# Kernel optimization log

Hardware: AMD Instinct MI355X
Metric: run time of the kernel (lower is better)

The kernel has to match this reference:

```python
import jax, jax.numpy as jnp
import numpy as np

D_MODEL = 1024
N_EXPERTS = 16384
N_HEADS = 8
TOP_K = 16
D_KEY = 128
N_SUB = int(np.sqrt(N_EXPERTS))  # 128
BN_EPS = 1e-5
RMS_EPS = 1e-6


def setup_inputs() -> dict:
    key = jax.random.key(0)
    ks = jax.random.split(key, 12)
    b, t = 2, 512
    hk = N_HEADS * D_KEY  # 1024
    s = 0.02
    return {
        "x": jax.random.normal(ks[0], (b, t, D_MODEL), dtype=jnp.float32),
        "wq": jax.random.normal(ks[1], (hk, D_MODEL), dtype=jnp.float32) * s,
        "bq": jnp.zeros((hk,), dtype=jnp.float32),
        "bn_w": jnp.ones((hk,), dtype=jnp.float32),
        "bn_b": jnp.zeros((hk,), dtype=jnp.float32),
        "bn_mean": jnp.zeros((hk,), dtype=jnp.float32),
        "bn_var": jnp.ones((hk,), dtype=jnp.float32),
        "sub_keys": jax.random.normal(ks[2], (2, N_SUB, D_KEY // 2), dtype=jnp.float32),
        "expert_weights": jax.random.normal(ks[3], (N_EXPERTS, D_KEY), dtype=jnp.float32),
        "wo": jax.random.normal(ks[4], (D_MODEL, hk), dtype=jnp.float32) * s,
        "bo": jnp.zeros((D_MODEL,), dtype=jnp.float32),
        "in_proj_w": jax.random.normal(ks[5], (3 * D_MODEL, D_MODEL), dtype=jnp.float32) * s,
        "in_proj_b": jnp.zeros((3 * D_MODEL,), dtype=jnp.float32),
        "attn_ow": jax.random.normal(ks[6], (D_MODEL, D_MODEL), dtype=jnp.float32) * s,
        "attn_ob": jnp.zeros((D_MODEL,), dtype=jnp.float32),
        "rms_w": jnp.ones((D_MODEL,), dtype=jnp.float32),
    }


def reference(x, wq, bq, bn_w, bn_b, bn_mean, bn_var, sub_keys, expert_weights,
              wo, bo, in_proj_w, in_proj_b, attn_ow, attn_ob, rms_w):
    b, t, d = x.shape
    h, dk = N_HEADS, D_KEY

    # ---- PEER query path ----
    q = jnp.einsum('btd,ed->bte', x, wq) + bq                       # (b,t,h*dk)
    # BatchNorm1d in eval mode with running stats
    q = (q - bn_mean) * jax.lax.rsqrt(bn_var + BN_EPS) * bn_w + bn_b
    q = q.reshape(b, t, h, dk)

    # ---- product-key top-k retrieval ----
    q1, q2 = q[..., : dk // 2], q[..., dk // 2 :]
    s1 = jnp.einsum('bthc,nc->bthn', q1, sub_keys[0])               # (b,t,h,N_SUB)
    s2 = jnp.einsum('bthc,nc->bthn', q2, sub_keys[1])
    # cartesian add; flat index = i1*N_SUB + i2 (matches torch view)
    scores = (s1[..., :, None] + s2[..., None, :]).reshape(b, t, h, N_SUB * N_SUB)
    _, idx = jax.lax.top_k(scores, TOP_K)                           # (b,t,h,k)

    # ---- gather experts, router softmax, weighted sum ----
    ew = expert_weights[idx]                                        # (b,t,h,k,dk)
    sim = jnp.einsum('bthd,bthkd->bthk', q, ew)
    rw = jax.nn.softmax(sim, axis=-1)
    out = jnp.einsum('bthk,bthkd->bthd', rw, ew).reshape(b, t, h * dk)
    out = jnp.einsum('bte,de->btd', out, wo) + bo                   # (b,t,d)

    # ---- multihead self-attention (torch nn.MultiheadAttention semantics) ----
    hd = d // h
    qkv = jnp.einsum('btd,ed->bte', x, in_proj_w) + in_proj_b       # (b,t,3d)
    qa, ka, va = jnp.split(qkv, 3, axis=-1)
    def heads(z):
        return z.reshape(b, t, h, hd).transpose(0, 2, 1, 3)         # (b,h,t,hd)
    qa, ka, va = heads(qa), heads(ka), heads(va)
    att = jax.nn.softmax(jnp.einsum('bhqe,bhke->bhqk', qa, ka) / np.sqrt(hd), axis=-1)
    ao = jnp.einsum('bhqk,bhke->bhqe', att, va).transpose(0, 2, 1, 3).reshape(b, t, d)
    ao = jnp.einsum('btd,ed->bte', ao, attn_ow) + attn_ob
    attn_weights = att.mean(axis=1)                                 # (b,t,t), averaged over heads

    # ---- residual + RMSNorm ----
    y = x + out + ao
    y = y * jax.lax.rsqrt(jnp.mean(y * y, axis=-1, keepdims=True) + RMS_EPS) * rms_w
    return y, attn_weights
```

## Files before the change

### kernel.cpp

```cpp
#include <hip/hip_runtime.h>
#include <hip/hip_bf16.h>
#include <math.h>

typedef __attribute__((ext_vector_type(8))) short bf16x8;
typedef __attribute__((ext_vector_type(4))) float f32x4;

__device__ inline short f2bf(float f) {
    __hip_bfloat16 h = __float2bfloat16(f);
    return *reinterpret_cast<short*>(&h);
}

__device__ inline unsigned int obits(float f) {
    unsigned int u = __float_as_uint(f);
    return (u & 0x80000000u) ? ~u : (u | 0x80000000u);
}

__global__ __launch_bounds__(256) void gemm_mfma64(
    const float* __restrict__ A, long lda, long sAb, long sAh,
    const float* __restrict__ B, long ldb, long sBb, long sBh,
    float* __restrict__ C, long ldc, long sCb, long sCh,
    int K, const float* __restrict__ bias, float scale, int hDiv)
{
    int bz = blockIdx.z;
    int bb = bz / hDiv, hh = bz % hDiv;
    A += bb * sAb + hh * sAh;
    B += bb * sBb + hh * sBh;
    C += bb * sCb + hh * sCh;
    int bm = blockIdx.y * 64, bn = blockIdx.x * 64;

    __shared__ __align__(16) short Asub[2][2048];
    __shared__ __align__(16) short Bsub[2][2048];

    int tid = threadIdx.x;
    int lane = tid & 63;
    int wave = tid >> 6;
    int wr = wave >> 1, wc = wave & 1;
    int l15 = lane & 15, l4 = lane >> 4;

    f32x4 acc[2][2] = {};

    int sr = tid >> 2;
    int sq = tid & 3;
    const float* gA = A + (long)(bm + sr) * lda + sq * 8;
    const float* gB = B + (long)(bn + sr) * ldb + sq * 8;
    int woff = (sr >> 4) * 512 + sq * 128 + (sr & 15) * 8;

    float4 a0 = *(const float4*)(gA);
    float4 a1 = *(const float4*)(gA + 4);
    float4 b0 = *(const float4*)(gB);
    float4 b1 = *(const float4*)(gB + 4);
    {
        bf16x8 ua, ub;
        ua[0]=f2bf(a0.x); ua[1]=f2bf(a0.y); ua[2]=f2bf(a0.z); ua[3]=f2bf(a0.w);
        ua[4]=f2bf(a1.x); ua[5]=f2bf(a1.y); ua[6]=f2bf(a1.z); ua[7]=f2bf(a1.w);
        ub[0]=f2bf(b0.x); ub[1]=f2bf(b0.y); ub[2]=f2bf(b0.z); ub[3]=f2bf(b0.w);
        ub[4]=f2bf(b1.x); ub[5]=f2bf(b1.y); ub[6]=f2bf(b1.z); ub[7]=f2bf(b1.w);
        *(bf16x8*)(Asub[0] + woff) = ua;
        *(bf16x8*)(Bsub[0] + woff) = ub;
    }
    if (K > 32) {
        a0 = *(const float4*)(gA + 32);
        a1 = *(const float4*)(gA + 36);
        b0 = *(const float4*)(gB + 32);
        b1 = *(const float4*)(gB + 36);
    }
    __syncthreads();

    int p = 0;
    for (int k0 = 0; k0 < K; k0 += 32) {
        bf16x8 af[2], bfr[2];
#pragma unroll
        for (int mi = 0; mi < 2; mi++)
            af[mi] = *(const bf16x8*)(Asub[p] + (wr * 2 + mi) * 512 + l4 * 128 + l15 * 8);
#pragma unroll
        for (int ni = 0; ni < 2; ni++)
            bfr[ni] = *(const bf16x8*)(Bsub[p] + (wc * 2 + ni) * 512 + l4 * 128 + l15 * 8);

        if (k0 + 32 < K) {
            bf16x8 ua, ub;
            ua[0]=f2bf(a0.x); ua[1]=f2bf(a0.y); ua[2]=f2bf(a0.z); ua[3]=f2bf(a0.w);
            ua[4]=f2bf(a1.x); ua[5]=f2bf(a1.y); ua[6]=f2bf(a1.z); ua[7]=f2bf(a1.w);
            ub[0]=f2bf(b0.x); ub[1]=f2bf(b0.y); ub[2]=f2bf(b0.z); ub[3]=f2bf(b0.w);
            ub[4]=f2bf(b1.x); ub[5]=f2bf(b1.y); ub[6]=f2bf(b1.z); ub[7]=f2bf(b1.w);
            *(bf16x8*)(Asub[p ^ 1] + woff) = ua;
            *(bf16x8*)(Bsub[p ^ 1] + woff) = ub;
            if (k0 + 64 < K) {
                a0 = *(const float4*)(gA + k0 + 64);
                a1 = *(const float4*)(gA + k0 + 68);
                b0 = *(const float4*)(gB + k0 + 64);
                b1 = *(const float4*)(gB + k0 + 68);
            }
        }

#pragma unroll
        for (int mi = 0; mi < 2; mi++)
#pragma unroll
            for (int ni = 0; ni < 2; ni++)
                acc[mi][ni] = __builtin_amdgcn_mfma_f32_16x16x32_bf16(
                    af[mi], bfr[ni], acc[mi][ni], 0, 0, 0);
        __syncthreads();
        p ^= 1;
    }

#pragma unroll
    for (int ni = 0; ni < 2; ni++) {
        int c = bn + wc * 32 + ni * 16 + l15;
        float bv = bias ? bias[c] : 0.f;
#pragma unroll
        for (int mi = 0; mi < 2; mi++) {
            int r0 = bm + wr * 32 + mi * 16 + l4 * 4;
#pragma unroll
            for (int e = 0; e < 4; e++)
                C[(long)(r0 + e) * ldc + c] = acc[mi][ni][e] * scale + bv;
        }
    }
}

__global__ __launch_bounds__(256) void sgemm_qproj(
    const float* __restrict__ A, const float* __restrict__ W,
    float* __restrict__ Q,
    const float* __restrict__ bq, const float* __restrict__ bn_w,
    const float* __restrict__ bn_b, const float* __restrict__ bn_mean,
    const float* __restrict__ bn_var)
{
    int bm = blockIdx.y * 64, bn = blockIdx.x * 64;
    __shared__ float As[32][64];
    __shared__ float Bs[32][64];
    int tid = threadIdx.x;
    int tx = tid & 15, ty = tid >> 4;
    int r = tid >> 2, q4 = tid & 3;
    float acc[4][4] = {{0.f}};

    const float* ga = A + (long)(bm + r) * 1024 + q4 * 8;
    const float* gb = W + (long)(bn + r) * 1024 + q4 * 8;

    float4 a0 = *(const float4*)(ga);
    float4 a1 = *(const float4*)(ga + 4);
    float4 b0 = *(const float4*)(gb);
    float4 b1 = *(const float4*)(gb + 4);

    for (int k0 = 0; k0 < 1024; k0 += 32) {
        __syncthreads();
        As[q4 * 8 + 0][r] = a0.x; As[q4 * 8 + 1][r] = a0.y;
        As[q4 * 8 + 2][r] = a0.z; As[q4 * 8 + 3][r] = a0.w;
        As[q4 * 8 + 4][r] = a1.x; As[q4 * 8 + 5][r] = a1.y;
        As[q4 * 8 + 6][r] = a1.z; As[q4 * 8 + 7][r] = a1.w;
        Bs[q4 * 8 + 0][r] = b0.x; Bs[q4 * 8 + 1][r] = b0.y;
        Bs[q4 * 8 + 2][r] = b0.z; Bs[q4 * 8 + 3][r] = b0.w;
        Bs[q4 * 8 + 4][r] = b1.x; Bs[q4 * 8 + 5][r] = b1.y;
        Bs[q4 * 8 + 6][r] = b1.z; Bs[q4 * 8 + 7][r] = b1.w;
        if (k0 + 32 < 1024) {
            a0 = *(const float4*)(ga + k0 + 32);
            a1 = *(const float4*)(ga + k0 + 36);
            b0 = *(const float4*)(gb + k0 + 32);
            b1 = *(const float4*)(gb + k0 + 36);
        }
        __syncthreads();
#pragma unroll
        for (int kk = 0; kk < 32; kk++) {
            float4 av = *(const float4*)&As[kk][ty * 4];
            float4 bv = *(const float4*)&Bs[kk][tx * 4];
            float a[4] = {av.x, av.y, av.z, av.w};
            float b[4] = {bv.x, bv.y, bv.z, bv.w};
#pragma unroll
            for (int i = 0; i < 4; i++)
#pragma unroll
                for (int j = 0; j < 4; j++)
                    acc[i][j] = fmaf(a[i], b[j], acc[i][j]);
        }
    }

#pragma unroll
    for (int j = 0; j < 4; j++) {
        int n = bn + tx * 4 + j;
        float s = rsqrtf(bn_var[n] + 1e-5f) * bn_w[n];
        float base = bq[n] - bn_mean[n];
        float bb = bn_b[n];
#pragma unroll
        for (int i = 0; i < 4; i++) {
            long m = bm + ty * 4 + i;
            Q[m * 1024 + n] = (acc[i][j] + base) * s + bb;
        }
    }
}

__global__ __launch_bounds__(256) void transpose_va(
    const float* __restrict__ qkv, float* __restrict__ vat)
{
    int z = blockIdx.z;
    int b = z >> 3, h = z & 7;
    int k0 = blockIdx.x * 32, n0 = blockIdx.y * 32;
    __shared__ float tile[32][33];
    int tx = threadIdx.x & 31, ty = threadIdx.x >> 5;
    const float* src = qkv + 2048 + (long)b * 1572864 + (long)h * 128;
#pragma unroll
    for (int i = 0; i < 4; i++)
        tile[ty + 8 * i][tx] = src[(long)(k0 + ty + 8 * i) * 3072 + n0 + tx];
    __syncthreads();
    float* dst = vat + (long)z * 65536;
#pragma unroll
    for (int i = 0; i < 4; i++)
        dst[(long)(n0 + ty + 8 * i) * 512 + k0 + tx] = tile[tx][ty + 8 * i];
}

__global__ __launch_bounds__(128) void peer_kernel(
    const float* __restrict__ q,
    const float* __restrict__ sub_keys,
    const float* __restrict__ ew,
    float* __restrict__ out)
{
    int th = blockIdx.x;
    int tid = threadIdx.x;

    __shared__ __align__(16) float qrow[128];
    __shared__ __align__(16) float s1s[128];
    __shared__ __align__(16) float s2s[128];
    __shared__ __align__(16) unsigned long long cks[256];
    __shared__ float tv1[16], tv2[16];
    __shared__ int   ti1[16], ti2[16];
    __shared__ int   part[100];
    __shared__ int   eid[16];
    __shared__ float simv[16];
    __shared__ float rw[16];

    qrow[tid] = q[(long)th * 128 + tid];
    __syncthreads();

    float a1 = 0.f, a2 = 0.f;
    {
        const float4* k1 = (const float4*)(sub_keys + tid * 64);
        const float4* k2 = (const float4*)(sub_keys + 8192 + tid * 64);
#pragma unroll 4
        for (int c = 0; c < 16; c++) {
            float4 q1 = *(const float4*)&qrow[4 * c];
            float4 q2 = *(const float4*)&qrow[64 + 4 * c];
            float4 v1 = k1[c], v2 = k2[c];
            a1 = fmaf(q1.x, v1.x, a1); a1 = fmaf(q1.y, v1.y, a1);
            a1 = fmaf(q1.z, v1.z, a1); a1 = fmaf(q1.w, v1.w, a1);
            a2 = fmaf(q2.x, v2.x, a2); a2 = fmaf(q2.y, v2.y, a2);
            a2 = fmaf(q2.z, v2.z, a2); a2 = fmaf(q2.w, v2.w, a2);
        }
    }
    s1s[tid] = a1;
    s2s[tid] = a2;
    __syncthreads();

    {
        int r1 = 0, r2 = 0;
        for (int j = 0; j < 128; j += 4) {
            float4 a = *(const float4*)&s1s[j];
            float4 b = *(const float4*)&s2s[j];
            r1 += (a.x > a1) || (a.x == a1 && j + 0 < tid);
            r1 += (a.y > a1) || (a.y == a1 && j + 1 < tid);
            r1 += (a.z > a1) || (a.z == a1 && j + 2 < tid);
            r1 += (a.w > a1) || (a.w == a1 && j + 3 < tid);
            r2 += (b.x > a2) || (b.x == a2 && j + 0 < tid);
            r2 += (b.y > a2) || (b.y == a2 && j + 1 < tid);
            r2 += (b.z > a2) || (b.z == a2 && j + 2 < tid);
            r2 += (b.w > a2) || (b.w == a2 && j + 3 < tid);
        }
        if (r1 < 16) { tv1[r1] = a1; ti1[r1] = tid; }
        if (r2 < 16) { tv2[r2] = a2; ti2[r2] = tid; }
    }
    __syncthreads();

    {
        int c0 = tid, c1 = tid + 128;
        float s0 = tv1[c0 >> 4] + tv2[c0 & 15];
        int e0 = ti1[c0 >> 4] * 128 + ti2[c0 & 15];
        cks[c0] = ((unsigned long long)obits(s0) << 32) | (unsigned)(16383 - e0);
        float s1v = tv1[c1 >> 4] + tv2[c1 & 15];
        int e1 = ti1[c1 >> 4] * 128 + ti2[c1 & 15];
        cks[c1] = ((unsigned long long)obits(s1v) << 32) | (unsigned)(16383 - e1);
    }
    __syncthreads();

    if (tid < 100) {
        int c = tid >> 1, h = tid & 1;
        int i, j;
        if      (c < 16) { i = 0; j = c; }
        else if (c < 24) { i = 1; j = c - 16; }
        else if (c < 29) { i = 2; j = c - 24; }
        else if (c < 33) { i = 3; j = c - 29; }
        else if (c < 36) { i = 4; j = c - 33; }
        else if (c < 38) { i = 5; j = c - 36; }
        else if (c < 40) { i = 6; j = c - 38; }
        else if (c < 42) { i = 7; j = c - 40; }
        else             { i = 8 + (c - 42); j = 0; }
        unsigned long long mk = cks[i * 16 + j];
        const ulonglong2* base = (const ulonglong2*)(cks + h * 128);
        int cnt = 0;
#pragma unroll 4
        for (int t = 0; t < 64; t++) {
            ulonglong2 kk = base[t];
            cnt += (kk.x > mk);
            cnt += (kk.y > mk);
        }
        part[tid] = cnt;
    }
    __syncthreads();
    if (tid < 50) {
        int r = part[2 * tid] + part[2 * tid + 1];
        if (r < 16) {
            int c = tid;
            int i, j;
            if      (c < 16) { i = 0; j = c; }
            else if (c < 24) { i = 1; j = c - 16; }
            else if (c < 29) { i = 2; j = c - 24; }
            else if (c < 33) { i = 3; j = c - 29; }
            else if (c < 36) { i = 4; j = c - 33; }
            else if (c < 38) { i = 5; j = c - 36; }
            else if (c < 40) { i = 6; j = c - 38; }
            else if (c < 42) { i = 7; j = c - 40; }
            else             { i = 8 + (c - 42); j = 0; }
            eid[r] = ti1[i] * 128 + ti2[j];
        }
    }
    __syncthreads();

    {
        int e = tid >> 3, g = tid & 7;
        const float4* e4 = (const float4*)(ew + (long)eid[e] * 128 + g * 16);
        const float4* qb = (const float4*)(qrow + g * 16);
        float acc = 0.f;
#pragma unroll
        for (int m = 0; m < 4; m++) {
            float4 v = e4[m];
            float4 qv = qb[m];
            acc = fmaf(qv.x, v.x, acc);
            acc = fmaf(qv.y, v.y, acc);
            acc = fmaf(qv.z, v.z, acc);
            acc = fmaf(qv.w, v.w, acc);
        }
        acc += __shfl_down(acc, 4);
        acc += __shfl_down(acc, 2);
        acc += __shfl_down(acc, 1);
        if (g == 0) simv[e] = acc;
    }
    __syncthreads();

    if (tid < 16) {
        float mx = simv[0];
#pragma unroll
        for (int k = 1; k < 16; k++) mx = fmaxf(mx, simv[k]);
        rw[tid] = expf(simv[tid] - mx);
    }
    __syncthreads();

    {
        float wsum = 0.f;
#pragma unroll
        for (int k = 0; k < 16; k++) wsum += rw[k];
        float inv = 1.f / wsum;
        float o = 0.f;
#pragma unroll
        for (int k = 0; k < 16; k++)
            o = fmaf(rw[k], ew[(long)eid[k] * 128 + tid], o);
        out[(long)th * 128 + tid] = o * inv;
    }
}

__global__ __launch_bounds__(256) void softmax_mean(
    float* __restrict__ att, float* __restrict__ outw)
{
    int blk = blockIdx.x;
    int b = blk >> 9, row = blk & 511;
    int tid = threadIdx.x;
    int w = tid >> 6, lane = tid & 63;

    __shared__ float msum[4][516];

#pragma unroll
    for (int pass = 0; pass < 2; pass++) {
        int h = w + pass * 4;
        long base = ((long)(b * 8 + h) * 512 + row) * 512 + lane * 8;
        float4 v0 = *(const float4*)(att + base);
        float4 v1 = *(const float4*)(att + base + 4);
        float m = fmaxf(fmaxf(fmaxf(v0.x, v0.y), fmaxf(v0.z, v0.w)),
                        fmaxf(fmaxf(v1.x, v1.y), fmaxf(v1.z, v1.w)));
#pragma unroll
        for (int off = 32; off > 0; off >>= 1)
            m = fmaxf(m, __shfl_xor(m, off));
        float e[8];
        e[0] = expf(v0.x - m); e[1] = expf(v0.y - m);
        e[2] = expf(v0.z - m); e[3] = expf(v0.w - m);
        e[4] = expf(v1.x - m); e[5] = expf(v1.y - m);
        e[6] = expf(v1.z - m); e[7] = expf(v1.w - m);
        float s = e[0] + e[1] + e[2] + e[3] + e[4] + e[5] + e[6] + e[7];
#pragma unroll
        for (int off = 32; off > 0; off >>= 1)
            s += __shfl_xor(s, off);
        float inv = 1.f / s;
        float4 p0 = make_float4(e[0] * inv, e[1] * inv, e[2] * inv, e[3] * inv);
        float4 p1 = make_float4(e[4] * inv, e[5] * inv, e[6] * inv, e[7] * inv);
        *(float4*)(att + base) = p0;
        *(float4*)(att + base + 4) = p1;
        int c = lane * 8;
        if (pass == 0) {
            msum[w][c + 0] = p0.x; msum[w][c + 1] = p0.y;
            msum[w][c + 2] = p0.z; msum[w][c + 3] = p0.w;
            msum[w][c + 4] = p1.x; msum[w][c + 5] = p1.y;
            msum[w][c + 6] = p1.z; msum[w][c + 7] = p1.w;
        } else {
            msum[w][c + 0] += p0.x; msum[w][c + 1] += p0.y;
            msum[w][c + 2] += p0.z; msum[w][c + 3] += p0.w;
            msum[w][c + 4] += p1.x; msum[w][c + 5] += p1.y;
            msum[w][c + 6] += p1.z; msum[w][c + 7] += p1.w;
        }
    }
    __syncthreads();
#pragma unroll
    for (int i = 0; i < 2; i++) {
        int c = tid + i * 256;
        float s = (msum[0][c] + msum[1][c] + msum[2][c] + msum[3][c]) * 0.125f;
        outw[(long)blk * 512 + c] = s;
    }
}

__global__ __launch_bounds__(256) void final_fuse(
    const float* __restrict__ x, const float* __restrict__ out2,
    const float* __restrict__ ao2, const float* __restrict__ rms_w,
    float* __restrict__ y)
{
    long base = (long)blockIdx.x * 1024;
    int tid = threadIdx.x;
    float v[4];
    float ss = 0.f;
#pragma unroll
    for (int i = 0; i < 4; i++) {
        int d = tid + i * 256;
        v[i] = x[base + d] + out2[base + d] + ao2[base + d];
        ss = fmaf(v[i], v[i], ss);
    }
    __shared__ float red[256];
    red[tid] = ss;
    __syncthreads();
    for (int st = 128; st > 0; st >>= 1) {
        if (tid < st) red[tid] += red[tid + st];
        __syncthreads();
    }
    float scale = rsqrtf(red[0] * (1.f / 1024.f) + 1e-6f);
#pragma unroll
    for (int i = 0; i < 4; i++) {
        int d = tid + i * 256;
        y[base + d] = v[i] * scale * rms_w[d];
    }
}

extern "C" void kernel_launch(void* const* d_in, const int* in_sizes, int n_in,
                              void* d_out, int out_size, void* d_ws, size_t ws_size,
                              hipStream_t stream)
{
    const float* x         = (const float*)d_in[0];
    const float* wq        = (const float*)d_in[1];
    const float* bq        = (const float*)d_in[2];
    const float* bn_w      = (const float*)d_in[3];
    const float* bn_b      = (const float*)d_in[4];
    const float* bn_mean   = (const float*)d_in[5];
    const float* bn_var    = (const float*)d_in[6];
    const float* sub_keys  = (const float*)d_in[7];
    const float* ew        = (const float*)d_in[8];
    const float* wo        = (const float*)d_in[9];
    const float* bo        = (const float*)d_in[10];
    const float* in_proj_w = (const float*)d_in[11];
    const float* in_proj_b = (const float*)d_in[12];
    const float* attn_ow   = (const float*)d_in[13];
    const float* attn_ob   = (const float*)d_in[14];
    const float* rms_w     = (const float*)d_in[15];
    float* out = (float*)d_out;

    float* ws   = (float*)d_ws;
    float* q    = ws;
    float* peer = ws + 1048576;
    float* out2 = ws + 2097152;
    float* qkv  = ws + 3145728;
    float* att  = ws + 6291456;
    float* ao   = ws + 10485760;
    float* ao2  = ws + 11534336;
    float* vat  = q;

    dim3 blk(256);

    sgemm_qproj<<<dim3(16, 16, 1), blk, 0, stream>>>(
        x, wq, q, bq, bn_w, bn_b, bn_mean, bn_var);

    peer_kernel<<<8192, 128, 0, stream>>>(q, sub_keys, ew, peer);

    gemm_mfma64<<<dim3(16, 16, 1), blk, 0, stream>>>(
        peer, 1024L, 0L, 0L, wo, 1024L, 0L, 0L, out2, 1024L, 0L, 0L,
        1024, bo, 1.0f, 1);

    gemm_mfma64<<<dim3(48, 16, 1), blk, 0, stream>>>(
        x, 1024L, 0L, 0L, in_proj_w, 1024L, 0L, 0L, qkv, 3072L, 0L, 0L,
        1024, in_proj_b, 1.0f, 1);

    transpose_va<<<dim3(16, 4, 16), blk, 0, stream>>>(qkv, vat);

    gemm_mfma64<<<dim3(8, 8, 16), blk, 0, stream>>>(
        qkv, 3072L, 1572864L, 128L,
        qkv + 1024, 3072L, 1572864L, 128L,
        att, 512L, 2097152L, 262144L,
        128, nullptr, 0.08838834764831845f, 8);

    softmax_mean<<<1024, 256, 0, stream>>>(att, out + 1048576);

    gemm_mfma64<<<dim3(2, 8, 16), blk, 0, stream>>>(
        att, 512L, 2097152L, 262144L,
        vat, 512L, 524288L, 65536L,
        ao, 1024L, 524288L, 128L,
        512, nullptr, 1.0f, 8);

    gemm_mfma64<<<dim3(16, 16, 1), blk, 0, stream>>>(
        ao, 1024L, 0L, 0L, attn_ow, 1024L, 0L, 0L, ao2, 1024L, 0L, 0L,
        1024, attn_ob, 1.0f, 1);

    final_fuse<<<1024, 256, 0, stream>>>(x, out2, ao2, rms_w, out);
}
```

Baseline: 316.2 us.

## Split-K with atomics for small GEMMs, smaller qproj tiles, packed-key top-k ranking

Adds a split-K MFMA GEMM that accumulates partial tiles into zeroed outputs with float atomics, and uses it for the wo, attention-V and out-projection GEMMs to raise block counts on under-filled grids. The biases move into the final fused RMSNorm kernel. The q-projection SGEMM now uses 32-row tiles to double its block count. The sub-key top-k rank now compares packed 64-bit value/index keys instead of float comparisons with index tie-breaks, and one loop is unrolled further. In exchange it adds three memset launches and atomic traffic, and the summation order becomes nondeterministic.

```diff
diff --git a/kernel.cpp b/kernel.cpp
--- a/kernel.cpp
+++ b/kernel.cpp
@@ -116,6 +116,107 @@
     }
 }
 
+__global__ __launch_bounds__(256) void gemm_mfma64_at(
+    const float* __restrict__ A, long lda, long sAb, long sAh,
+    const float* __restrict__ B, long ldb, long sBb, long sBh,
+    float* __restrict__ C, long ldc, long sCb, long sCh,
+    int Ktile, float scale, int hDiv, int nbz)
+{
+    int z = blockIdx.z;
+    int bz = z % nbz, ks = z / nbz;
+    int bb = bz / hDiv, hh = bz % hDiv;
+    A += bb * sAb + hh * sAh + (long)ks * Ktile;
+    B += bb * sBb + hh * sBh + (long)ks * Ktile;
+    C += bb * sCb + hh * sCh;
+    int bm = blockIdx.y * 64, bn = blockIdx.x * 64;
+
+    __shared__ __align__(16) short Asub[2][2048];
+    __shared__ __align__(16) short Bsub[2][2048];
+
+    int tid = threadIdx.x;
+    int lane = tid & 63;
+    int wave = tid >> 6;
+    int wr = wave >> 1, wc = wave & 1;
+    int l15 = lane & 15, l4 = lane >> 4;
+
+    f32x4 acc[2][2] = {};
+
+    int sr = tid >> 2;
+    int sq = tid & 3;
+    const float* gA = A + (long)(bm + sr) * lda + sq * 8;
+    const float* gB = B + (long)(bn + sr) * ldb + sq * 8;
+    int woff = (sr >> 4) * 512 + sq * 128 + (sr & 15) * 8;
+
+    float4 a0 = *(const float4*)(gA);
+    float4 a1 = *(const float4*)(gA + 4);
+    float4 b0 = *(const float4*)(gB);
+    float4 b1 = *(const float4*)(gB + 4);
+    {
+        bf16x8 ua, ub;
+        ua[0]=f2bf(a0.x); ua[1]=f2bf(a0.y); ua[2]=f2bf(a0.z); ua[3]=f2bf(a0.w);
+        ua[4]=f2bf(a1.x); ua[5]=f2bf(a1.y); ua[6]=f2bf(a1.z); ua[7]=f2bf(a1.w);
+        ub[0]=f2bf(b0.x); ub[1]=f2bf(b0.y); ub[2]=f2bf(b0.z); ub[3]=f2bf(b0.w);
+        ub[4]=f2bf(b1.x); ub[5]=f2bf(b1.y); ub[6]=f2bf(b1.z); ub[7]=f2bf(b1.w);
+        *(bf16x8*)(Asub[0] + woff) = ua;
+        *(bf16x8*)(Bsub[0] + woff) = ub;
+    }
+    if (Ktile > 32) {
+        a0 = *(const float4*)(gA + 32);
+        a1 = *(const float4*)(gA + 36);
+        b0 = *(const float4*)(gB + 32);
+        b1 = *(const float4*)(gB + 36);
+    }
+    __syncthreads();
+
+    int p = 0;
+    for (int k0 = 0; k0 < Ktile; k0 += 32) {
+        bf16x8 af[2], bfr[2];
+#pragma unroll
+        for (int mi = 0; mi < 2; mi++)
+            af[mi] = *(const bf16x8*)(Asub[p] + (wr * 2 + mi) * 512 + l4 * 128 + l15 * 8);
+#pragma unroll
+        for (int ni = 0; ni < 2; ni++)
+            bfr[ni] = *(const bf16x8*)(Bsub[p] + (wc * 2 + ni) * 512 + l4 * 128 + l15 * 8);
+
+        if (k0 + 32 < Ktile) {
+            bf16x8 ua, ub;
+            ua[0]=f2bf(a0.x); ua[1]=f2bf(a0.y); ua[2]=f2bf(a0.z); ua[3]=f2bf(a0.w);
+            ua[4]=f2bf(a1.x); ua[5]=f2bf(a1.y); ua[6]=f2bf(a1.z); ua[7]=f2bf(a1.w);
+            ub[0]=f2bf(b0.x); ub[1]=f2bf(b0.y); ub[2]=f2bf(b0.z); ub[3]=f2bf(b0.w);
+            ub[4]=f2bf(b1.x); ub[5]=f2bf(b1.y); ub[6]=f2bf(b1.z); ub[7]=f2bf(b1.w);
+            *(bf16x8*)(Asub[p ^ 1] + woff) = ua;
+            *(bf16x8*)(Bsub[p ^ 1] + woff) = ub;
+            if (k0 + 64 < Ktile) {
+                a0 = *(const float4*)(gA + k0 + 64);
+                a1 = *(const float4*)(gA + k0 + 68);
+                b0 = *(const float4*)(gB + k0 + 64);
+                b1 = *(const float4*)(gB + k0 + 68);
+            }
+        }
+
+#pragma unroll
+        for (int mi = 0; mi < 2; mi++)
+#pragma unroll
+            for (int ni = 0; ni < 2; ni++)
+                acc[mi][ni] = __builtin_amdgcn_mfma_f32_16x16x32_bf16(
+                    af[mi], bfr[ni], acc[mi][ni], 0, 0, 0);
+        __syncthreads();
+        p ^= 1;
+    }
+
+#pragma unroll
+    for (int ni = 0; ni < 2; ni++) {
+        int c = bn + wc * 32 + ni * 16 + l15;
+#pragma unroll
+        for (int mi = 0; mi < 2; mi++) {
+            int r0 = bm + wr * 32 + mi * 16 + l4 * 4;
+#pragma unroll
+            for (int e = 0; e < 4; e++)
+                atomicAdd(&C[(long)(r0 + e) * ldc + c], acc[mi][ni][e] * scale);
+        }
+    }
+}
+
 __global__ __launch_bounds__(256) void sgemm_qproj(
     const float* __restrict__ A, const float* __restrict__ W,
     float* __restrict__ Q,
@@ -123,47 +224,44 @@
     const float* __restrict__ bn_b, const float* __restrict__ bn_mean,
     const float* __restrict__ bn_var)
 {
-    int bm = blockIdx.y * 64, bn = blockIdx.x * 64;
-    __shared__ float As[32][64];
+    int bm = blockIdx.y * 32, bn = blockIdx.x * 64;
+    __shared__ float As[32][34];
     __shared__ float Bs[32][64];
     int tid = threadIdx.x;
     int tx = tid & 15, ty = tid >> 4;
-    int r = tid >> 2, q4 = tid & 3;
-    float acc[4][4] = {{0.f}};
-
-    const float* ga = A + (long)(bm + r) * 1024 + q4 * 8;
-    const float* gb = W + (long)(bn + r) * 1024 + q4 * 8;
+    int ar = tid >> 3, ak = (tid & 7) * 4;
+    int br = tid & 63, bk = (tid >> 6) * 8;
+    float acc[2][4] = {{0.f}};
+
+    const float* ga = A + (long)(bm + ar) * 1024 + ak;
+    const float* gb = W + (long)(bn + br) * 1024 + bk;
 
     float4 a0 = *(const float4*)(ga);
-    float4 a1 = *(const float4*)(ga + 4);
     float4 b0 = *(const float4*)(gb);
     float4 b1 = *(const float4*)(gb + 4);
 
     for (int k0 = 0; k0 < 1024; k0 += 32) {
         __syncthreads();
-        As[q4 * 8 + 0][r] = a0.x; As[q4 * 8 + 1][r] = a0.y;
-        As[q4 * 8 + 2][r] = a0.z; As[q4 * 8 + 3][r] = a0.w;
-        As[q4 * 8 + 4][r] = a1.x; As[q4 * 8 + 5][r] = a1.y;
-        As[q4 * 8 + 6][r] = a1.z; As[q4 * 8 + 7][r] = a1.w;
-        Bs[q4 * 8 + 0][r] = b0.x; Bs[q4 * 8 + 1][r] = b0.y;
-        Bs[q4 * 8 + 2][r] = b0.z; Bs[q4 * 8 + 3][r] = b0.w;
-        Bs[q4 * 8 + 4][r] = b1.x; Bs[q4 * 8 + 5][r] = b1.y;
-        Bs[q4 * 8 + 6][r] = b1.z; Bs[q4 * 8 + 7][r] = b1.w;
+        As[ak + 0][ar] = a0.x; As[ak + 1][ar] = a0.y;
+        As[ak + 2][ar] = a0.z; As[ak + 3][ar] = a0.w;
+        Bs[bk + 0][br] = b0.x; Bs[bk + 1][br] = b0.y;
+        Bs[bk + 2][br] = b0.z; Bs[bk + 3][br] = b0.w;
+        Bs[bk + 4][br] = b1.x; Bs[bk + 5][br] = b1.y;
+        Bs[bk + 6][br] = b1.z; Bs[bk + 7][br] = b1.w;
         if (k0 + 32 < 1024) {
             a0 = *(const float4*)(ga + k0 + 32);
-            a1 = *(const float4*)(ga + k0 + 36);
             b0 = *(const float4*)(gb + k0 + 32);
             b1 = *(const float4*)(gb + k0 + 36);
         }
         __syncthreads();
 #pragma unroll
         for (int kk = 0; kk < 32; kk++) {
-            float4 av = *(const float4*)&As[kk][ty * 4];
+            float2 av = *(const float2*)&As[kk][ty * 2];
             float4 bv = *(const float4*)&Bs[kk][tx * 4];
-            float a[4] = {av.x, av.y, av.z, av.w};
+            float a[2] = {av.x, av.y};
             float b[4] = {bv.x, bv.y, bv.z, bv.w};
 #pragma unroll
-            for (int i = 0; i < 4; i++)
+            for (int i = 0; i < 2; i++)
 #pragma unroll
                 for (int j = 0; j < 4; j++)
                     acc[i][j] = fmaf(a[i], b[j], acc[i][j]);
@@ -177,8 +275,8 @@
         float base = bq[n] - bn_mean[n];
         float bb = bn_b[n];
 #pragma unroll
-        for (int i = 0; i < 4; i++) {
-            long m = bm + ty * 4 + i;
+        for (int i = 0; i < 2; i++) {
+            long m = bm + ty * 2 + i;
             Q[m * 1024 + n] = (acc[i][j] + base) * s + bb;
         }
     }
@@ -213,8 +311,8 @@
     int tid = threadIdx.x;
 
     __shared__ __align__(16) float qrow[128];
-    __shared__ __align__(16) float s1s[128];
-    __shared__ __align__(16) float s2s[128];
+    __shared__ __align__(16) unsigned long long k1s[128];
+    __shared__ __align__(16) unsigned long long k2s[128];
     __shared__ __align__(16) unsigned long long cks[256];
     __shared__ float tv1[16], tv2[16];
     __shared__ int   ti1[16], ti2[16];
@@ -241,23 +339,20 @@
             a2 = fmaf(q2.z, v2.z, a2); a2 = fmaf(q2.w, v2.w, a2);
         }
     }
-    s1s[tid] = a1;
-    s2s[tid] = a2;
+    unsigned long long key1 = ((unsigned long long)obits(a1) << 32) | (unsigned)(127 - tid);
+    unsigned long long key2 = ((unsigned long long)obits(a2) << 32) | (unsigned)(127 - tid);
+    k1s[tid] = key1;
+    k2s[tid] = key2;
     __syncthreads();
 
     {
         int r1 = 0, r2 = 0;
-        for (int j = 0; j < 128; j += 4) {
-            float4 a = *(const float4*)&s1s[j];
-            float4 b = *(const float4*)&s2s[j];
-            r1 += (a.x > a1) || (a.x == a1 && j + 0 < tid);
-            r1 += (a.y > a1) || (a.y == a1 && j + 1 < tid);
-            r1 += (a.z > a1) || (a.z == a1 && j + 2 < tid);
-            r1 += (a.w > a1) || (a.w == a1 && j + 3 < tid);
-            r2 += (b.x > a2) || (b.x == a2 && j + 0 < tid);
-            r2 += (b.y > a2) || (b.y == a2 && j + 1 < tid);
-            r2 += (b.z > a2) || (b.z == a2 && j + 2 < tid);
-            r2 += (b.w > a2) || (b.w == a2 && j + 3 < tid);
+#pragma unroll 8
+        for (int j = 0; j < 128; j += 2) {
+            ulonglong2 ka = *(const ulonglong2*)&k1s[j];
+            ulonglong2 kb = *(const ulonglong2*)&k2s[j];
+            r1 += (ka.x > key1) + (ka.y > key1);
+            r2 += (kb.x > key2) + (kb.y > key2);
         }
         if (r1 < 16) { tv1[r1] = a1; ti1[r1] = tid; }
         if (r2 < 16) { tv2[r2] = a2; ti2[r2] = tid; }
@@ -290,7 +385,7 @@
         unsigned long long mk = cks[i * 16 + j];
         const ulonglong2* base = (const ulonglong2*)(cks + h * 128);
         int cnt = 0;
-#pragma unroll 4
+#pragma unroll 8
         for (int t = 0; t < 64; t++) {
             ulonglong2 kk = base[t];
             cnt += (kk.x > mk);
@@ -420,6 +515,7 @@
 __global__ __launch_bounds__(256) void final_fuse(
     const float* __restrict__ x, const float* __restrict__ out2,
     const float* __restrict__ ao2, const float* __restrict__ rms_w,
+    const float* __restrict__ bo, const float* __restrict__ attn_ob,
     float* __restrict__ y)
 {
     long base = (long)blockIdx.x * 1024;
@@ -429,7 +525,7 @@
 #pragma unroll
     for (int i = 0; i < 4; i++) {
         int d = tid + i * 256;
-        v[i] = x[base + d] + out2[base + d] + ao2[base + d];
+        v[i] = x[base + d] + out2[base + d] + ao2[base + d] + bo[d] + attn_ob[d];
         ss = fmaf(v[i], v[i], ss);
     }
     __shared__ float red[256];
@@ -481,14 +577,18 @@
 
     dim3 blk(256);
 
-    sgemm_qproj<<<dim3(16, 16, 1), blk, 0, stream>>>(
+    hipMemsetAsync(out2, 0, 4194304, stream);
+    hipMemsetAsync(ao,   0, 4194304, stream);
+    hipMemsetAsync(ao2,  0, 4194304, stream);
+
+    sgemm_qproj<<<dim3(16, 32, 1), blk, 0, stream>>>(
         x, wq, q, bq, bn_w, bn_b, bn_mean, bn_var);
 
     peer_kernel<<<8192, 128, 0, stream>>>(q, sub_keys, ew, peer);
 
-    gemm_mfma64<<<dim3(16, 16, 1), blk, 0, stream>>>(
+    gemm_mfma64_at<<<dim3(16, 16, 4), blk, 0, stream>>>(
         peer, 1024L, 0L, 0L, wo, 1024L, 0L, 0L, out2, 1024L, 0L, 0L,
-        1024, bo, 1.0f, 1);
+        256, 1.0f, 1, 1);
 
     gemm_mfma64<<<dim3(48, 16, 1), blk, 0, stream>>>(
         x, 1024L, 0L, 0L, in_proj_w, 1024L, 0L, 0L, qkv, 3072L, 0L, 0L,
@@ -504,15 +604,15 @@
 
     softmax_mean<<<1024, 256, 0, stream>>>(att, out + 1048576);
 
-    gemm_mfma64<<<dim3(2, 8, 16), blk, 0, stream>>>(
+    gemm_mfma64_at<<<dim3(2, 8, 32), blk, 0, stream>>>(
         att, 512L, 2097152L, 262144L,
         vat, 512L, 524288L, 65536L,
         ao, 1024L, 524288L, 128L,
-        512, nullptr, 1.0f, 8);
-
-    gemm_mfma64<<<dim3(16, 16, 1), blk, 0, stream>>>(
+        256, 1.0f, 8, 16);
+
+    gemm_mfma64_at<<<dim3(16, 16, 4), blk, 0, stream>>>(
         ao, 1024L, 0L, 0L, attn_ow, 1024L, 0L, 0L, ao2, 1024L, 0L, 0L,
-        1024, attn_ob, 1.0f, 1);
-
-    final_fuse<<<1024, 256, 0, stream>>>(x, out2, ao2, rms_w, out);
-}
+        256, 1.0f, 1, 1);
+
+    final_fuse<<<1024, 256, 0, stream>>>(x, out2, ao2, rms_w, bo, attn_ob, out);
+}
```

Result: slower. 327.7 us (+3.6%).
